# Performance work log

Hardware: AMD Instinct MI355X
Metric: run time of the kernel (lower is better)

## Reference

```python
import jax, jax.numpy as jnp
import numpy as np

FS = 4  # filter_size: input3 has FS*FS channels (DAIN default)


def setup_inputs() -> dict:
    key = jax.random.key(0)
    k1, k2, k3 = jax.random.split(key, 3)
    B, C, H, W = 4, 3, 544, 960
    input1 = jax.random.normal(k1, (B, C, H, W), jnp.float32)          # image
    input2 = jax.random.normal(k2, (B, 2, H, W), jnp.float32)          # flow (x, y)
    input3 = jax.random.uniform(k3, (B, FS * FS, H, W), jnp.float32)   # per-pixel filters
    return {"input1": input1, "input2": input2, "input3": input3}


def _filter_interp(input1, input2, input3):
    B, C, H, W = input1.shape
    fs = int(round(np.sqrt(input3.shape[1])))
    fx = input2[:, 0]  # [B,H,W]
    fy = input2[:, 1]
    xs = jnp.arange(W, dtype=input1.dtype)
    ys = jnp.arange(H, dtype=input1.dtype)
    x2 = xs[None, None, :] + fx   # sample x position per output pixel
    y2 = ys[None, :, None] + fy
    mask = ((x2 >= 0) & (y2 >= 0) & (x2 <= W - 1) & (y2 <= H - 1)
            & (jnp.abs(fx) < W / 2.0) & (jnp.abs(fy) < H / 2.0))
    x2c = jnp.clip(x2, 0.0, W - 1)
    y2c = jnp.clip(y2, 0.0, H - 1)
    ix = jnp.floor(x2c).astype(jnp.int32)   # int(x2), x2>=0 inside mask
    iy = jnp.floor(y2c).astype(jnp.int32)
    alpha = (x2c - ix).astype(input1.dtype)  # fractional part
    beta = (y2c - iy).astype(input1.dtype)
    ixL = ix + 1 - fs // 2                   # top-left tap of filter window
    iyT = iy + 1 - fs // 2

    img = input1.reshape(B, C, H * W)

    def gather(yi, xi):
        # yi, xi: int [B,H,W] (already clamped) -> [B,C,H,W]
        idx = (yi * W + xi).reshape(B, 1, H * W)
        g = jnp.take_along_axis(img, jnp.broadcast_to(idx, (B, C, H * W)), axis=2)
        return g.reshape(B, C, H, W)

    # bilinear blend weights of the four shifted window sums (TL,TR,BL,BR)
    wa = ((1 - alpha) * (1 - beta))[:, None]
    wb = (alpha * (1 - beta))[:, None]
    wc = ((1 - alpha) * beta)[:, None]
    wd = (alpha * beta)[:, None]

    out = jnp.zeros_like(input1)
    for j in range(fs):          # fixed small filter window, unrolled
        yT = jnp.clip(iyT + j, 0, H - 1)
        yB = jnp.clip(iyT + j + 1, 0, H - 1)
        for i in range(fs):
            xL = jnp.clip(ixL + i, 0, W - 1)
            xR = jnp.clip(ixL + i + 1, 0, W - 1)
            samp = (wa * gather(yT, xL) + wb * gather(yT, xR)
                    + wc * gather(yB, xL) + wd * gather(yB, xR))
            out = out + samp * input3[:, j * fs + i][:, None]
    return out * mask[:, None].astype(input1.dtype)


def reference(input1, input2, input3):
    return _filter_interp(input1, input2, input3)
```

## Files before the change

kernel.cpp:

```cpp
#include <hip/hip_runtime.h>


#define BB 4
#define HH 544
#define WW 960
#define HW (HH * WW)

#define BX 64
#define BY 8
#define MARG 6
#define TW (BX + 2 * MARG)
#define TH (BY + 2 * MARG)
#define RS4 (TW + 1)

typedef float v4f __attribute__((ext_vector_type(4)));

__global__ __launch_bounds__(256) void filt_interp_kernel(
    const float* __restrict__ img,
    const float* __restrict__ flow,
    const float* __restrict__ filt,
    float* __restrict__ out)
{
    __shared__ v4f tile[TH * RS4];

    const int tid = threadIdx.x;
    const int x0 = blockIdx.x * BX;
    const int y0 = blockIdx.y * BY;
    const int b  = blockIdx.z;
    const int tx0 = x0 - MARG;
    const int ty0 = y0 - MARG;

    const float* ibase = img + (size_t)b * 3 * HW;
    for (int li = tid; li < TH * TW; li += 256) {
        int vr = li / TW;
        int vc = li - vr * TW;
        int gy = min(max(ty0 + vr, 0), HH - 1);
        int gx = min(max(tx0 + vc, 0), WW - 1);
        const float* ip = ibase + gy * WW + gx;
        v4f t;
        t.x = ip[0];
        t.y = ip[HW];
        t.z = ip[2 * HW];
        t.w = 0.0f;
        tile[vr * RS4 + vc] = t;
    }
    __syncthreads();

    const int xp = tid & 31;
    const int yr = tid >> 5;
    const int xb = x0 + xp;
    const int y = y0 + yr;
    const int pix = y * WW + xb;

    const float* flp = flow + (size_t)b * 2 * HW + pix;
    float fxk[2], fyk[2];
    fxk[0] = __builtin_nontemporal_load(flp);
    fxk[1] = __builtin_nontemporal_load(flp + 32);
    fyk[0] = __builtin_nontemporal_load(flp + HW);
    fyk[1] = __builtin_nontemporal_load(flp + HW + 32);

    const float* fp = filt + (size_t)b * 16 * HW + pix;
    float w3k[2][16];
#pragma unroll
    for (int t = 0; t < 16; t++) {
        w3k[0][t] = __builtin_nontemporal_load(fp + (size_t)t * HW);
        w3k[1][t] = __builtin_nontemporal_load(fp + (size_t)t * HW + 32);
    }

    float res[2][3];

#pragma unroll
    for (int k = 0; k < 2; k++) {
        const int xk = xb + 32 * k;
        float fx = fxk[k];
        float fy = fyk[k];
        float x2 = (float)xk + fx;
        float y2 = (float)y + fy;
        bool m = (x2 >= 0.0f) && (y2 >= 0.0f) &&
                 (x2 <= (float)(WW - 1)) && (y2 <= (float)(HH - 1)) &&
                 (fabsf(fx) < (float)WW * 0.5f) && (fabsf(fy) < (float)HH * 0.5f);
        float x2c = fminf(fmaxf(x2, 0.0f), (float)(WW - 1));
        float y2c = fminf(fmaxf(y2, 0.0f), (float)(HH - 1));
        int ix = (int)floorf(x2c);
        int iy = (int)floorf(y2c);
        float alpha = x2c - (float)ix;
        float beta  = y2c - (float)iy;
        int ixL = ix - 1;
        int iyT = iy - 1;
        float mf = m ? 1.0f : 0.0f;
        float wa = (1.0f - alpha) * (1.0f - beta) * mf;
        float wb = alpha * (1.0f - beta) * mf;
        float wc = (1.0f - alpha) * beta * mf;
        float wd = alpha * beta * mf;

        float W5[5][5];
#pragma unroll
        for (int r = 0; r < 5; r++)
#pragma unroll
            for (int c = 0; c < 5; c++) W5[r][c] = 0.0f;

#pragma unroll
        for (int j = 0; j < 4; j++) {
#pragma unroll
            for (int i = 0; i < 4; i++) {
                float w3 = w3k[k][j * 4 + i];
                W5[j][i]         += wa * w3;
                W5[j][i + 1]     += wb * w3;
                W5[j + 1][i]     += wc * w3;
                W5[j + 1][i + 1] += wd * w3;
            }
        }

        bool ok = (iyT >= ty0) && (iyT + 4 <= ty0 + TH - 1) &&
                  (ixL >= tx0) && (ixL + 4 <= tx0 + TW - 1);

        if (ok) {
            int base = (iyT - ty0) * RS4 + (ixL - tx0);
            v4f acc = {0.0f, 0.0f, 0.0f, 0.0f};
#pragma unroll
            for (int r = 0; r < 5; r++) {
#pragma unroll
                for (int c = 0; c < 5; c++) {
                    acc += W5[r][c] * tile[base + r * RS4 + c];
                }
            }
            res[k][0] = acc.x;
            res[k][1] = acc.y;
            res[k][2] = acc.z;
        } else {
            float ax = 0.0f, ay = 0.0f, az = 0.0f;
            int cx[5], ry[5];
#pragma unroll
            for (int q = 0; q < 5; q++) {
                cx[q] = min(max(ixL + q, 0), WW - 1);
                ry[q] = min(max(iyT + q, 0), HH - 1);
            }
#pragma unroll
            for (int r = 0; r < 5; r++) {
                const float* rowp = ibase + ry[r] * WW;
#pragma unroll
                for (int c = 0; c < 5; c++) {
                    float w = W5[r][c];
                    const float* p = rowp + cx[c];
                    ax = fmaf(w, p[0], ax);
                    ay = fmaf(w, p[HW], ay);
                    az = fmaf(w, p[2 * HW], az);
                }
            }
            res[k][0] = ax;
            res[k][1] = ay;
            res[k][2] = az;
        }
    }

    float* ob = out + (size_t)b * 3 * HW + pix;
#pragma unroll
    for (int ch = 0; ch < 3; ch++) {
        __builtin_nontemporal_store(res[0][ch], ob + (size_t)ch * HW);
        __builtin_nontemporal_store(res[1][ch], ob + (size_t)ch * HW + 32);
    }
}

extern "C" void kernel_launch(void* const* d_in, const int* in_sizes, int n_in,
                              void* d_out, int out_size, void* d_ws, size_t ws_size,
                              hipStream_t stream) {
    const float* img  = (const float*)d_in[0];
    const float* flow = (const float*)d_in[1];
    const float* filt = (const float*)d_in[2];
    float* out = (float*)d_out;

    dim3 grid(WW / BX, HH / BY, BB);
    filt_interp_kernel<<<grid, 256, 0, stream>>>(img, flow, filt, out);
}
```

Measured before the change: 218.6 us.

## Swizzle workgroup order across XCDs and tidy address and weight computation

Switches from a 3D grid to a 1D grid and remaps block IDs so that each of the 8 XCDs gets a contiguous chunk of tiles. Neighbouring tiles then share one XCD's L2 for the halo reads. Address arithmetic now uses base pointers plus 32-bit offsets, which may allow cheaper buffer addressing. The 5x5 weight build now initialises entries directly instead of zeroing them first. The mapping depends on NWG being divisible by 8, which holds for these sizes.

```diff
diff --git a/kernel.cpp b/kernel.cpp
--- a/kernel.cpp
+++ b/kernel.cpp
@@ -13,6 +13,11 @@
 #define TH (BY + 2 * MARG)
 #define RS4 (TW + 1)
 
+#define GXB (WW / BX)
+#define GYB (HH / BY)
+#define NWG (GXB * GYB * BB)
+#define CHUNK (NWG / 8)
+
 typedef float v4f __attribute__((ext_vector_type(4)));
 
 __global__ __launch_bounds__(256) void filt_interp_kernel(
@@ -23,24 +28,32 @@
 {
     __shared__ v4f tile[TH * RS4];
 
+    const int wg  = blockIdx.x;
+    const int swz = (wg & 7) * CHUNK + (wg >> 3);
+    const int b   = swz / (GXB * GYB);
+    const int rem = swz - b * (GXB * GYB);
+    const int by  = rem / GXB;
+    const int bx  = rem - by * GXB;
+
     const int tid = threadIdx.x;
-    const int x0 = blockIdx.x * BX;
-    const int y0 = blockIdx.y * BY;
-    const int b  = blockIdx.z;
+    const int x0 = bx * BX;
+    const int y0 = by * BY;
     const int tx0 = x0 - MARG;
     const int ty0 = y0 - MARG;
 
-    const float* ibase = img + (size_t)b * 3 * HW;
+    const float* ib0 = img + (size_t)b * 3 * HW;
+    const float* ib1 = ib0 + HW;
+    const float* ib2 = ib0 + 2 * HW;
     for (int li = tid; li < TH * TW; li += 256) {
         int vr = li / TW;
         int vc = li - vr * TW;
         int gy = min(max(ty0 + vr, 0), HH - 1);
         int gx = min(max(tx0 + vc, 0), WW - 1);
-        const float* ip = ibase + gy * WW + gx;
+        int gi = gy * WW + gx;
         v4f t;
-        t.x = ip[0];
-        t.y = ip[HW];
-        t.z = ip[2 * HW];
+        t.x = ib0[gi];
+        t.y = ib1[gi];
+        t.z = ib2[gi];
         t.w = 0.0f;
         tile[vr * RS4 + vc] = t;
     }
@@ -52,19 +65,19 @@
     const int y = y0 + yr;
     const int pix = y * WW + xb;
 
-    const float* flp = flow + (size_t)b * 2 * HW + pix;
+    const float* fb = flow + (size_t)b * 2 * HW;
     float fxk[2], fyk[2];
-    fxk[0] = __builtin_nontemporal_load(flp);
-    fxk[1] = __builtin_nontemporal_load(flp + 32);
-    fyk[0] = __builtin_nontemporal_load(flp + HW);
-    fyk[1] = __builtin_nontemporal_load(flp + HW + 32);
+    fxk[0] = __builtin_nontemporal_load(fb + pix);
+    fxk[1] = __builtin_nontemporal_load(fb + pix + 32);
+    fyk[0] = __builtin_nontemporal_load(fb + HW + pix);
+    fyk[1] = __builtin_nontemporal_load(fb + HW + pix + 32);
 
-    const float* fp = filt + (size_t)b * 16 * HW + pix;
+    const float* ftb = filt + (size_t)b * 16 * HW;
     float w3k[2][16];
 #pragma unroll
     for (int t = 0; t < 16; t++) {
-        w3k[0][t] = __builtin_nontemporal_load(fp + (size_t)t * HW);
-        w3k[1][t] = __builtin_nontemporal_load(fp + (size_t)t * HW + 32);
+        w3k[0][t] = __builtin_nontemporal_load(ftb + (size_t)t * HW + pix);
+        w3k[1][t] = __builtin_nontemporal_load(ftb + (size_t)t * HW + pix + 32);
     }
 
     float res[2][3];
@@ -95,19 +108,17 @@
 
         float W5[5][5];
 #pragma unroll
-        for (int r = 0; r < 5; r++)
-#pragma unroll
-            for (int c = 0; c < 5; c++) W5[r][c] = 0.0f;
-
-#pragma unroll
         for (int j = 0; j < 4; j++) {
 #pragma unroll
             for (int i = 0; i < 4; i++) {
                 float w3 = w3k[k][j * 4 + i];
-                W5[j][i]         += wa * w3;
-                W5[j][i + 1]     += wb * w3;
-                W5[j + 1][i]     += wc * w3;
-                W5[j + 1][i + 1] += wd * w3;
+                if (j == 0 && i == 0) W5[j][i] = wa * w3;
+                else                  W5[j][i] = fmaf(wa, w3, W5[j][i]);
+                if (j == 0)           W5[j][i + 1] = wb * w3;
+                else                  W5[j][i + 1] = fmaf(wb, w3, W5[j][i + 1]);
+                if (i == 0)           W5[j + 1][i] = wc * w3;
+                else                  W5[j + 1][i] = fmaf(wc, w3, W5[j + 1][i]);
+                W5[j + 1][i + 1] = wd * w3;
             }
         }
 
@@ -137,14 +148,14 @@
             }
 #pragma unroll
             for (int r = 0; r < 5; r++) {
-                const float* rowp = ibase + ry[r] * WW;
+                int rowb = ry[r] * WW;
 #pragma unroll
                 for (int c = 0; c < 5; c++) {
                     float w = W5[r][c];
-                    const float* p = rowp + cx[c];
-                    ax = fmaf(w, p[0], ax);
-                    ay = fmaf(w, p[HW], ay);
-                    az = fmaf(w, p[2 * HW], az);
+                    int gi = rowb + cx[c];
+                    ax = fmaf(w, ib0[gi], ax);
+                    ay = fmaf(w, ib1[gi], ay);
+                    az = fmaf(w, ib2[gi], az);
                 }
             }
             res[k][0] = ax;
@@ -153,11 +164,11 @@
         }
     }
 
-    float* ob = out + (size_t)b * 3 * HW + pix;
+    float* ob = out + (size_t)b * 3 * HW;
 #pragma unroll
     for (int ch = 0; ch < 3; ch++) {
-        __builtin_nontemporal_store(res[0][ch], ob + (size_t)ch * HW);
-        __builtin_nontemporal_store(res[1][ch], ob + (size_t)ch * HW + 32);
+        __builtin_nontemporal_store(res[0][ch], ob + (size_t)ch * HW + pix);
+        __builtin_nontemporal_store(res[1][ch], ob + (size_t)ch * HW + pix + 32);
     }
 }
 
@@ -169,6 +180,5 @@
     const float* filt = (const float*)d_in[2];
     float* out = (float*)d_out;
 
-    dim3 grid(WW / BX, HH / BY, BB);
-    filt_interp_kernel<<<grid, 256, 0, stream>>>(img, flow, filt, out);
+    filt_interp_kernel<<<dim3(NWG), 256, 0, stream>>>(img, flow, filt, out);
 }
```

Result: no change. 216.3 us, median of 2 (-1.1%).
